# Kernel tuning notes

Hardware: AMD Instinct MI355X
Metric: run time of the kernel (lower is better)

Reference implementation:

```python
import jax, jax.numpy as jnp
import numpy as np

N = 50000      # nodes
E = 800000     # edges (before self loops)
IN_DIM = 256
HID = 64       # per-head hidden dim
HEADS = 4
NEG_SLOPE = 0.2


def setup_inputs() -> dict:
    key = jax.random.key(0)
    k1, k2, k3, k4, k5, k6 = jax.random.split(key, 6)
    x = jax.random.normal(k1, (N, IN_DIM), dtype=jnp.float32)
    edge_index = jax.random.randint(k2, (2, E), 0, N, dtype=jnp.int64)
    # GATConv params (PyG layout): lin weight, att_src, att_dst, bias
    W = jax.random.normal(k3, (IN_DIM, HEADS * HID), dtype=jnp.float32) / np.sqrt(IN_DIM)
    att_src = jax.random.normal(k4, (HEADS, HID), dtype=jnp.float32) / np.sqrt(HID)
    att_dst = jax.random.normal(k5, (HEADS, HID), dtype=jnp.float32) / np.sqrt(HID)
    bias = jnp.zeros((HEADS * HID,), dtype=jnp.float32)
    return {"x": x, "edge_index": edge_index, "W": W,
            "att_src": att_src, "att_dst": att_dst, "bias": bias}


def _gat_forward(x, edge_index, W, att_src, att_dst, bias):
    n = x.shape[0]
    # linear projection per head: [N, H, F]
    h = (x @ W).reshape(n, HEADS, HID)
    # per-node attention logits (computed once on nodes, then gathered)
    a_src = jnp.einsum('nhf,hf->nh', h, att_src)  # [N, H]
    a_dst = jnp.einsum('nhf,hf->nh', h, att_dst)  # [N, H]
    # add self loops (PyG default add_self_loops=True)
    loop = jnp.arange(n, dtype=edge_index.dtype)
    src = jnp.concatenate([edge_index[0], loop])  # [E+N]
    dst = jnp.concatenate([edge_index[1], loop])  # [E+N]
    # edge attention logits with LeakyReLU
    e = jax.nn.leaky_relu(a_src[src] + a_dst[dst], NEG_SLOPE)  # [E+N, H]
    # segment softmax over incoming edges of each destination node
    m = jax.ops.segment_max(e, dst, num_segments=n)            # [N, H]
    num = jnp.exp(e - m[dst])                                  # [E+N, H]
    denom = jax.ops.segment_sum(num, dst, num_segments=n)      # [N, H]
    alpha = num / denom[dst]                                   # [E+N, H]
    # scatter-aggregate weighted source features
    msg = alpha[:, :, None] * h[src]                           # [E+N, H, F]
    out = jax.ops.segment_sum(msg, dst, num_segments=n)        # [N, H, F]
    out = out.reshape(n, HEADS * HID) + bias
    # GraphEncoder.forward: ReLU then Dropout (dropout=0 -> identity)
    return jax.nn.relu(out)


def reference(x, edge_index, W, att_src, att_dst, bias):
    return _gat_forward(x, edge_index, W, att_src, att_dst, bias)
```

## Files before the change

### kernel.cpp

```cpp
#include <hip/hip_runtime.h>
#include <hip/hip_bf16.h>

#define N_NODES 50000
#define N_EDGES 800000
#define TOT_EDGES (N_EDGES + N_NODES)
#define IN_DIM 256
#define OUT_DIM 256
#define HEADS 4
#define NEG_SLOPE 0.2f
#define CAP 96

#define FBLK 256
#define NT   1563
#define LDS_STRIDE 264

typedef __bf16 bf16x8 __attribute__((ext_vector_type(8)));
typedef __bf16 bf16x4 __attribute__((ext_vector_type(4)));
typedef float f32x4 __attribute__((ext_vector_type(4)));

__device__ __forceinline__ float b2f(unsigned short u) {
    union { float f; unsigned int i; } v; v.i = ((unsigned int)u) << 16; return v.f;
}

struct Args {
    const float* x; const int* ei; const float* W;
    const float* att_s; const float* att_d; const float* bias;
    float* out;
    __bf16* Wt; __bf16* h; float* a_src; float* a_dst;
    int* counts; int* ell;
};

__global__ void k_wt(Args A) {
    int k = blockIdx.x;
    int n = threadIdx.x;
    A.Wt[(size_t)n * IN_DIM + k] = (__bf16)A.W[(size_t)k * OUT_DIM + n];
    int idx = blockIdx.x * 256 + threadIdx.x;
    if (idx < N_NODES) A.counts[idx] = 0;
}

__global__ __launch_bounds__(512, 2) void k_gemm_fill(Args A) {
    __shared__ __bf16 xs[32 * LDS_STRIDE];
    __shared__ float  lg[2][8][32];
    const int t = threadIdx.x;

    if (blockIdx.x >= FBLK) {
        const int tile = blockIdx.x - FBLK;
        const int wave = t >> 6;
        const int lane = t & 63;
        const int cc   = lane & 15;
        const int quad = lane >> 4;
        const int n0   = wave * 32;
        const __bf16* __restrict__ Wt = A.Wt;
        const float4* __restrict__ x4 = (const float4*)A.x;

        bf16x8 Bf[8][2];
#pragma unroll
        for (int kk = 0; kk < 8; ++kk)
#pragma unroll
            for (int f = 0; f < 2; ++f)
                Bf[kk][f] = *(const bf16x8*)(Wt
                    + (size_t)(n0 + f * 16 + cc) * IN_DIM + kk * 32 + quad * 8);
        float as0 = A.att_s[n0 + cc], as1 = A.att_s[n0 + 16 + cc];
        float ad0 = A.att_d[n0 + cc], ad1 = A.att_d[n0 + 16 + cc];

        float4 st[4];
#pragma unroll
        for (int i = 0; i < 4; ++i) {
            int f = i * 512 + t;
            int row = f >> 6, c4 = f & 63;
            int grow = tile * 32 + row; if (grow >= N_NODES) grow = N_NODES - 1;
            st[i] = x4[(size_t)grow * 64 + c4];
        }
#pragma unroll
        for (int i = 0; i < 4; ++i) {
            int f = i * 512 + t;
            int row = f >> 6, c4 = f & 63;
            bf16x4 o = { (__bf16)st[i].x, (__bf16)st[i].y, (__bf16)st[i].z, (__bf16)st[i].w };
            *(bf16x4*)&xs[row * LDS_STRIDE + c4 * 4] = o;
        }
        __syncthreads();

        f32x4 acc[2][2];
#pragma unroll
        for (int mt = 0; mt < 2; ++mt)
#pragma unroll
            for (int f = 0; f < 2; ++f) acc[mt][f] = (f32x4){0.f, 0.f, 0.f, 0.f};
#pragma unroll
        for (int kk = 0; kk < 8; ++kk) {
#pragma unroll
            for (int mt = 0; mt < 2; ++mt) {
                bf16x8 a = *(const bf16x8*)&xs[(mt * 16 + cc) * LDS_STRIDE + kk * 32 + quad * 8];
                acc[mt][0] = __builtin_amdgcn_mfma_f32_16x16x32_bf16(a, Bf[kk][0], acc[mt][0], 0, 0, 0);
                acc[mt][1] = __builtin_amdgcn_mfma_f32_16x16x32_bf16(a, Bf[kk][1], acc[mt][1], 0, 0, 0);
            }
        }

#pragma unroll
        for (int mt = 0; mt < 2; ++mt) {
#pragma unroll
            for (int r = 0; r < 4; ++r) {
                float pS = acc[mt][0][r] * as0 + acc[mt][1][r] * as1;
                float pD = acc[mt][0][r] * ad0 + acc[mt][1][r] * ad1;
#pragma unroll
                for (int o = 8; o >= 1; o >>= 1) {
                    pS += __shfl_xor(pS, o, 64);
                    pD += __shfl_xor(pD, o, 64);
                }
                if (cc == 0) {
                    lg[0][wave][mt * 16 + quad * 4 + r] = pS;
                    lg[1][wave][mt * 16 + quad * 4 + r] = pD;
                }
            }
        }
        __syncthreads();

#pragma unroll
        for (int mt = 0; mt < 2; ++mt)
#pragma unroll
            for (int f = 0; f < 2; ++f)
#pragma unroll
                for (int r = 0; r < 4; ++r)
                    xs[(mt * 16 + quad * 4 + r) * LDS_STRIDE + n0 + f * 16 + cc] =
                        (__bf16)acc[mt][f][r];
        if (t < 256) {
            int td = t & 127;
            int row = td >> 2, head = td & 3;
            int grow = tile * 32 + row;
            if (grow < N_NODES) {
                int sd = t >> 7;
                float v = lg[sd][2 * head][row] + lg[sd][2 * head + 1][row];
                float* dst = sd == 0 ? A.a_src : A.a_dst;
                dst[grow * 4 + head] = v;
            }
        }
        __syncthreads();

#pragma unroll
        for (int i = 0; i < 2; ++i) {
            int idx = i * 512 + t;
            int row = idx >> 5, c8 = idx & 31;
            int grow = tile * 32 + row;
            if (grow < N_NODES)
                *(bf16x8*)(A.h + (size_t)grow * OUT_DIM + c8 * 8) =
                    *(const bf16x8*)&xs[row * LDS_STRIDE + c8 * 8];
        }
    } else {
        int nz = 0;
        for (int i = t; i < 1024; i += 512)
            if (A.ei[2 * i + 1] != 0) nz++;
        bool is64 = (__syncthreads_count(nz) == 0);
        const long long* ei64 = (const long long*)A.ei;
        for (int i = blockIdx.x * 512 + t; i < TOT_EDGES; i += FBLK * 512) {
            int s, d;
            if (i < N_EDGES) {
                if (is64) { s = (int)ei64[i]; d = (int)ei64[N_EDGES + i]; }
                else      { s = A.ei[i];      d = A.ei[N_EDGES + i]; }
            } else {
                s = d = i - N_EDGES;
            }
            int pos = atomicAdd(&A.counts[d], 1);
            if (pos < CAP) A.ell[(size_t)d * CAP + pos] = s;
        }
    }
}

__global__ __launch_bounds__(256) void k_agg(Args A) {
    __shared__ float lds_all[4][CAP][4];
    int wave = threadIdx.x >> 6, lane = threadIdx.x & 63;
    int node = blockIdx.x * 4 + wave;
    if (node >= N_NODES) return;
    float (*lds)[4] = lds_all[wave];

    int base = node * CAP;
    int deg  = A.counts[node];
    if (deg > CAP) deg = CAP;
    const float4* as4 = (const float4*)A.a_src;
    float4 ad = ((const float4*)A.a_dst)[node];

    float4 smv = {0.f, 0.f, 0.f, 0.f};
    for (int e = lane; e < deg; e += 64) {
        int s = A.ell[base + e];
        float4 av = as4[s];
        float4 l;
        l.x = av.x + ad.x; l.x = l.x > 0.f ? l.x : NEG_SLOPE * l.x;
        l.y = av.y + ad.y; l.y = l.y > 0.f ? l.y : NEG_SLOPE * l.y;
        l.z = av.z + ad.z; l.z = l.z > 0.f ? l.z : NEG_SLOPE * l.z;
        l.w = av.w + ad.w; l.w = l.w > 0.f ? l.w : NEG_SLOPE * l.w;
        float4 e4;
        e4.x = __expf(l.x); e4.y = __expf(l.y);
        e4.z = __expf(l.z); e4.w = __expf(l.w);
        smv.x += e4.x; smv.y += e4.y; smv.z += e4.z; smv.w += e4.w;
        lds[e][0] = e4.x; lds[e][1] = e4.y; lds[e][2] = e4.z; lds[e][3] = e4.w;
    }
    int padEnd = (deg + 3) & ~3;
    for (int e = deg + lane; e < padEnd; e += 64) {
        lds[e][0] = 0.f; lds[e][1] = 0.f; lds[e][2] = 0.f; lds[e][3] = 0.f;
    }
#pragma unroll
    for (int o = 32; o >= 1; o >>= 1) {
        smv.x += __shfl_xor(smv.x, o, 64);
        smv.y += __shfl_xor(smv.y, o, 64);
        smv.z += __shfl_xor(smv.z, o, 64);
        smv.w += __shfl_xor(smv.w, o, 64);
    }

    int head = lane >> 4;
    float smh = head == 0 ? smv.x : head == 1 ? smv.y : head == 2 ? smv.z : smv.w;
    float inv_d = 1.f / smh;

    float acc0 = 0.f, acc1 = 0.f, acc2 = 0.f, acc3 = 0.f;
    const unsigned short* hs = reinterpret_cast<const unsigned short*>(A.h);
    int rEnd = padEnd;
    for (int e = 0; e < rEnd; e += 4) {
        int s0 = A.ell[base + e];
        int s1 = A.ell[base + ((e + 1 < deg) ? e + 1 : 0)];
        int s2 = A.ell[base + ((e + 2 < deg) ? e + 2 : 0)];
        int s3 = A.ell[base + ((e + 3 < deg) ? e + 3 : 0)];
        float al0 = lds[e][head];
        float al1 = lds[e + 1][head];
        float al2 = lds[e + 2][head];
        float al3 = lds[e + 3][head];
        ushort4 h0 = *(const ushort4*)(hs + (size_t)s0 * OUT_DIM + lane * 4);
        ushort4 h1 = *(const ushort4*)(hs + (size_t)s1 * OUT_DIM + lane * 4);
        ushort4 h2 = *(const ushort4*)(hs + (size_t)s2 * OUT_DIM + lane * 4);
        ushort4 h3 = *(const ushort4*)(hs + (size_t)s3 * OUT_DIM + lane * 4);
        acc0 += al0 * b2f(h0.x) + al1 * b2f(h1.x) + al2 * b2f(h2.x) + al3 * b2f(h3.x);
        acc1 += al0 * b2f(h0.y) + al1 * b2f(h1.y) + al2 * b2f(h2.y) + al3 * b2f(h3.y);
        acc2 += al0 * b2f(h0.z) + al1 * b2f(h1.z) + al2 * b2f(h2.z) + al3 * b2f(h3.z);
        acc3 += al0 * b2f(h0.w) + al1 * b2f(h1.w) + al2 * b2f(h2.w) + al3 * b2f(h3.w);
    }

    float4 bv = ((const float4*)A.bias)[lane];
    f32x4 o4;
    float v0 = acc0 * inv_d + bv.x;
    float v1 = acc1 * inv_d + bv.y;
    float v2 = acc2 * inv_d + bv.z;
    float v3 = acc3 * inv_d + bv.w;
    o4[0] = v0 > 0.f ? v0 : 0.f;
    o4[1] = v1 > 0.f ? v1 : 0.f;
    o4[2] = v2 > 0.f ? v2 : 0.f;
    o4[3] = v3 > 0.f ? v3 : 0.f;
    __builtin_nontemporal_store(o4, (f32x4*)A.out + (size_t)node * 64 + lane);
}

extern "C" void kernel_launch(void* const* d_in, const int* in_sizes, int n_in,
                              void* d_out, int out_size, void* d_ws, size_t ws_size,
                              hipStream_t stream) {
    (void)out_size; (void)ws_size;
    const void* p_x = nullptr; const void* p_ei = nullptr; const void* p_W = nullptr;
    const void* p_small[3] = {nullptr, nullptr, nullptr}; int nsmall = 0;
    for (int i = 0; i < n_in; ++i) {
        switch (in_sizes[i]) {
            case N_NODES * IN_DIM:      p_x = d_in[i]; break;
            case 2 * N_EDGES:           p_ei = d_in[i]; break;
            case IN_DIM * OUT_DIM:      p_W = d_in[i]; break;
            case OUT_DIM:               if (nsmall < 3) p_small[nsmall++] = d_in[i]; break;
            default: break;
        }
    }
    if (!p_x)  p_x  = d_in[0];
    if (!p_ei) p_ei = d_in[1];
    if (!p_W)  p_W  = d_in[2];
    if (nsmall < 3) { p_small[0] = d_in[3]; p_small[1] = d_in[4]; p_small[2] = d_in[5]; }

    char* ws = (char*)d_ws;
    size_t off = 0;
    auto alloc = [&](size_t bytes) -> void* {
        void* p = ws + off;
        off = (off + bytes + 255) & ~(size_t)255;
        return p;
    };
    Args A;
    A.Wt      = (__bf16*)alloc((size_t)IN_DIM * OUT_DIM * 2);
    A.h       = (__bf16*)alloc((size_t)N_NODES * OUT_DIM * 2);
    A.a_src   = (float*)alloc((size_t)N_NODES * HEADS * 4);
    A.a_dst   = (float*)alloc((size_t)N_NODES * HEADS * 4);
    A.counts  = (int*)alloc((size_t)N_NODES * 4);
    A.ell     = (int*)alloc((size_t)N_NODES * CAP * 4);

    A.x     = (const float*)p_x;
    A.ei    = (const int*)p_ei;
    A.W     = (const float*)p_W;
    A.att_s = (const float*)p_small[0];
    A.att_d = (const float*)p_small[1];
    A.bias  = (const float*)p_small[2];
    A.out   = (float*)d_out;

    k_wt<<<dim3(IN_DIM), dim3(OUT_DIM), 0, stream>>>(A);
    k_gemm_fill<<<dim3(FBLK + NT), dim3(512), 0, stream>>>(A);
    k_agg<<<dim3((N_NODES + 3) / 4), dim3(256), 0, stream>>>(A);
}
```

Baseline: 241.7 us.

## Store h head-major and split aggregation per head across blocks

The projected features h are now written in a head-major layout [HEADS][N][64]. The aggregation kernel launches one block group per head, so each wave handles one node and one head. Within a wave, four lane groups each gather a different edge's 128-byte row and are then reduced with shuffles. The aim is a smaller per-head working set for the random gathers, better cache locality, and more parallelism, at the cost of reading the ELL adjacency and computing softmax sums four times per node.

```diff
diff --git a/kernel.cpp b/kernel.cpp
--- a/kernel.cpp
+++ b/kernel.cpp
@@ -12,6 +12,7 @@
 
 #define FBLK 256
 #define NT   1563
+#define NBN  12500
 #define LDS_STRIDE 264
 
 typedef __bf16 bf16x8 __attribute__((ext_vector_type(8)));
@@ -26,7 +27,8 @@
     const float* x; const int* ei; const float* W;
     const float* att_s; const float* att_d; const float* bias;
     float* out;
-    __bf16* Wt; __bf16* h; float* a_src; float* a_dst;
+    __bf16* Wt; __bf16* h;
+    float* a_src; float* a_dst;
     int* counts; int* ell;
 };
 
@@ -139,9 +141,10 @@
         for (int i = 0; i < 2; ++i) {
             int idx = i * 512 + t;
             int row = idx >> 5, c8 = idx & 31;
+            int hd  = c8 >> 3, d8 = c8 & 7;
             int grow = tile * 32 + row;
             if (grow < N_NODES)
-                *(bf16x8*)(A.h + (size_t)grow * OUT_DIM + c8 * 8) =
+                *(bf16x8*)(A.h + ((size_t)hd * N_NODES + grow) * 64 + d8 * 8) =
                     *(const bf16x8*)&xs[row * LDS_STRIDE + c8 * 8];
         }
     } else {
@@ -165,82 +168,65 @@
 }
 
 __global__ __launch_bounds__(256) void k_agg(Args A) {
-    __shared__ float lds_all[4][CAP][4];
-    int wave = threadIdx.x >> 6, lane = threadIdx.x & 63;
-    int node = blockIdx.x * 4 + wave;
+    __shared__ float alp_all[4][CAP];
+    const int wave = threadIdx.x >> 6, lane = threadIdx.x & 63;
+    const int head = blockIdx.x / NBN;
+    const int nb   = blockIdx.x % NBN;
+    const int node = nb * 4 + wave;
     if (node >= N_NODES) return;
-    float (*lds)[4] = lds_all[wave];
-
-    int base = node * CAP;
-    int deg  = A.counts[node];
+    float* alp = alp_all[wave];
+
+    const int base = node * CAP;
+    int deg = A.counts[node];
     if (deg > CAP) deg = CAP;
-    const float4* as4 = (const float4*)A.a_src;
-    float4 ad = ((const float4*)A.a_dst)[node];
-
-    float4 smv = {0.f, 0.f, 0.f, 0.f};
+    const float adh = A.a_dst[node * 4 + head];
+
+    float sm = 0.f;
     for (int e = lane; e < deg; e += 64) {
         int s = A.ell[base + e];
-        float4 av = as4[s];
-        float4 l;
-        l.x = av.x + ad.x; l.x = l.x > 0.f ? l.x : NEG_SLOPE * l.x;
-        l.y = av.y + ad.y; l.y = l.y > 0.f ? l.y : NEG_SLOPE * l.y;
-        l.z = av.z + ad.z; l.z = l.z > 0.f ? l.z : NEG_SLOPE * l.z;
-        l.w = av.w + ad.w; l.w = l.w > 0.f ? l.w : NEG_SLOPE * l.w;
-        float4 e4;
-        e4.x = __expf(l.x); e4.y = __expf(l.y);
-        e4.z = __expf(l.z); e4.w = __expf(l.w);
-        smv.x += e4.x; smv.y += e4.y; smv.z += e4.z; smv.w += e4.w;
-        lds[e][0] = e4.x; lds[e][1] = e4.y; lds[e][2] = e4.z; lds[e][3] = e4.w;
+        float l = A.a_src[s * 4 + head] + adh;
+        l = l > 0.f ? l : NEG_SLOPE * l;
+        float al = __expf(l);
+        sm += al;
+        alp[e] = al;
     }
     int padEnd = (deg + 3) & ~3;
-    for (int e = deg + lane; e < padEnd; e += 64) {
-        lds[e][0] = 0.f; lds[e][1] = 0.f; lds[e][2] = 0.f; lds[e][3] = 0.f;
-    }
-#pragma unroll
-    for (int o = 32; o >= 1; o >>= 1) {
-        smv.x += __shfl_xor(smv.x, o, 64);
-        smv.y += __shfl_xor(smv.y, o, 64);
-        smv.z += __shfl_xor(smv.z, o, 64);
-        smv.w += __shfl_xor(smv.w, o, 64);
-    }
-
-    int head = lane >> 4;
-    float smh = head == 0 ? smv.x : head == 1 ? smv.y : head == 2 ? smv.z : smv.w;
-    float inv_d = 1.f / smh;
-
-    float acc0 = 0.f, acc1 = 0.f, acc2 = 0.f, acc3 = 0.f;
-    const unsigned short* hs = reinterpret_cast<const unsigned short*>(A.h);
-    int rEnd = padEnd;
-    for (int e = 0; e < rEnd; e += 4) {
-        int s0 = A.ell[base + e];
-        int s1 = A.ell[base + ((e + 1 < deg) ? e + 1 : 0)];
-        int s2 = A.ell[base + ((e + 2 < deg) ? e + 2 : 0)];
-        int s3 = A.ell[base + ((e + 3 < deg) ? e + 3 : 0)];
-        float al0 = lds[e][head];
-        float al1 = lds[e + 1][head];
-        float al2 = lds[e + 2][head];
-        float al3 = lds[e + 3][head];
-        ushort4 h0 = *(const ushort4*)(hs + (size_t)s0 * OUT_DIM + lane * 4);
-        ushort4 h1 = *(const ushort4*)(hs + (size_t)s1 * OUT_DIM + lane * 4);
-        ushort4 h2 = *(const ushort4*)(hs + (size_t)s2 * OUT_DIM + lane * 4);
-        ushort4 h3 = *(const ushort4*)(hs + (size_t)s3 * OUT_DIM + lane * 4);
-        acc0 += al0 * b2f(h0.x) + al1 * b2f(h1.x) + al2 * b2f(h2.x) + al3 * b2f(h3.x);
-        acc1 += al0 * b2f(h0.y) + al1 * b2f(h1.y) + al2 * b2f(h2.y) + al3 * b2f(h3.y);
-        acc2 += al0 * b2f(h0.z) + al1 * b2f(h1.z) + al2 * b2f(h2.z) + al3 * b2f(h3.z);
-        acc3 += al0 * b2f(h0.w) + al1 * b2f(h1.w) + al2 * b2f(h2.w) + al3 * b2f(h3.w);
-    }
-
-    float4 bv = ((const float4*)A.bias)[lane];
-    f32x4 o4;
-    float v0 = acc0 * inv_d + bv.x;
-    float v1 = acc1 * inv_d + bv.y;
-    float v2 = acc2 * inv_d + bv.z;
-    float v3 = acc3 * inv_d + bv.w;
-    o4[0] = v0 > 0.f ? v0 : 0.f;
-    o4[1] = v1 > 0.f ? v1 : 0.f;
-    o4[2] = v2 > 0.f ? v2 : 0.f;
-    o4[3] = v3 > 0.f ? v3 : 0.f;
-    __builtin_nontemporal_store(o4, (f32x4*)A.out + (size_t)node * 64 + lane);
+    for (int e = deg + lane; e < padEnd; e += 64) alp[e] = 0.f;
+#pragma unroll
+    for (int o = 32; o >= 1; o >>= 1) sm += __shfl_xor(sm, o, 64);
+    const float inv_d = 1.f / sm;
+
+    const int grp = lane >> 4, d16 = lane & 15;
+    const unsigned short* __restrict__ hH =
+        (const unsigned short*)A.h + (size_t)head * N_NODES * 64;
+    float a0 = 0.f, a1 = 0.f, a2 = 0.f, a3 = 0.f;
+    for (int e0 = 0; e0 < padEnd; e0 += 4) {
+        int e = e0 + grp;
+        int s = (e < deg) ? A.ell[base + e] : 0;
+        float al = alp[e];
+        ushort4 hv = *(const ushort4*)(hH + (size_t)s * 64 + d16 * 4);
+        a0 += al * b2f(hv.x); a1 += al * b2f(hv.y);
+        a2 += al * b2f(hv.z); a3 += al * b2f(hv.w);
+    }
+#pragma unroll
+    for (int o = 32; o >= 16; o >>= 1) {
+        a0 += __shfl_xor(a0, o, 64); a1 += __shfl_xor(a1, o, 64);
+        a2 += __shfl_xor(a2, o, 64); a3 += __shfl_xor(a3, o, 64);
+    }
+    if (grp == 0) {
+        float4 bv = *(const float4*)(A.bias + head * 64 + d16 * 4);
+        float v0 = a0 * inv_d + bv.x;
+        float v1 = a1 * inv_d + bv.y;
+        float v2 = a2 * inv_d + bv.z;
+        float v3 = a3 * inv_d + bv.w;
+        f32x4 o4;
+        o4[0] = v0 > 0.f ? v0 : 0.f;
+        o4[1] = v1 > 0.f ? v1 : 0.f;
+        o4[2] = v2 > 0.f ? v2 : 0.f;
+        o4[3] = v3 > 0.f ? v3 : 0.f;
+        __builtin_nontemporal_store(o4,
+            (f32x4*)(A.out + (size_t)node * OUT_DIM + head * 64) + d16);
+    }
 }
 
 extern "C" void kernel_launch(void* const* d_in, const int* in_sizes, int n_in,
@@ -288,5 +274,5 @@
 
     k_wt<<<dim3(IN_DIM), dim3(OUT_DIM), 0, stream>>>(A);
     k_gemm_fill<<<dim3(FBLK + NT), dim3(512), 0, stream>>>(A);
-    k_agg<<<dim3((N_NODES + 3) / 4), dim3(256), 0, stream>>>(A);
-}
+    k_agg<<<dim3(HEADS * NBN), dim3(256), 0, stream>>>(A);
+}
```

Result: slower. 286.6 us (+18.6%).

## Fuse all three kernels into one persistent cooperative kernel with grid syncs

Applied to the files above, without the earlier changes.

Replaces the three launches (weight transpose/count init, GEMM plus edge fill, aggregation) with a single cooperative persistent kernel that separates phases with grid-wide syncs and loops over tiles and node groups. The aim is to remove launch gaps and tail effects between kernels. In exchange, the ELL fill and the GEMM, which used to run concurrently, now run one after the other. The grid is capped at 1024 blocks, and launch_bounds(512,8) may force register spills in the GEMM phase, which holds 16 bf16x8 B fragments per thread.

```diff
diff --git a/kernel.cpp b/kernel.cpp
--- a/kernel.cpp
+++ b/kernel.cpp
@@ -1,5 +1,8 @@
 #include <hip/hip_runtime.h>
 #include <hip/hip_bf16.h>
+#include <hip/hip_cooperative_groups.h>
+
+namespace cg = cooperative_groups;
 
 #define N_NODES 50000
 #define N_EDGES 800000
@@ -10,7 +13,6 @@
 #define NEG_SLOPE 0.2f
 #define CAP 96
 
-#define FBLK 256
 #define NT   1563
 #define LDS_STRIDE 264
 
@@ -26,131 +28,37 @@
     const float* x; const int* ei; const float* W;
     const float* att_s; const float* att_d; const float* bias;
     float* out;
-    __bf16* Wt; __bf16* h; float* a_src; float* a_dst;
+    __bf16* Wt; __bf16* h;
+    float* a_src; float* a_dst;
     int* counts; int* ell;
 };
 
-__global__ void k_wt(Args A) {
-    int k = blockIdx.x;
-    int n = threadIdx.x;
-    A.Wt[(size_t)n * IN_DIM + k] = (__bf16)A.W[(size_t)k * OUT_DIM + n];
-    int idx = blockIdx.x * 256 + threadIdx.x;
-    if (idx < N_NODES) A.counts[idx] = 0;
-}
-
-__global__ __launch_bounds__(512, 2) void k_gemm_fill(Args A) {
-    __shared__ __bf16 xs[32 * LDS_STRIDE];
-    __shared__ float  lg[2][8][32];
+__global__ __launch_bounds__(512, 8) void k_mega(Args A) {
+    __shared__ __align__(16) unsigned char smem[18944];
+    __bf16* xs = (__bf16*)smem;
+    float (*lg)[8][32] = (float(*)[8][32])(smem + 16896);
+    float (*alds)[CAP][4] = (float(*)[CAP][4])smem;
+
     const int t = threadIdx.x;
-
-    if (blockIdx.x >= FBLK) {
-        const int tile = blockIdx.x - FBLK;
-        const int wave = t >> 6;
-        const int lane = t & 63;
-        const int cc   = lane & 15;
-        const int quad = lane >> 4;
-        const int n0   = wave * 32;
-        const __bf16* __restrict__ Wt = A.Wt;
-        const float4* __restrict__ x4 = (const float4*)A.x;
-
-        bf16x8 Bf[8][2];
-#pragma unroll
-        for (int kk = 0; kk < 8; ++kk)
-#pragma unroll
-            for (int f = 0; f < 2; ++f)
-                Bf[kk][f] = *(const bf16x8*)(Wt
-                    + (size_t)(n0 + f * 16 + cc) * IN_DIM + kk * 32 + quad * 8);
-        float as0 = A.att_s[n0 + cc], as1 = A.att_s[n0 + 16 + cc];
-        float ad0 = A.att_d[n0 + cc], ad1 = A.att_d[n0 + 16 + cc];
-
-        float4 st[4];
-#pragma unroll
-        for (int i = 0; i < 4; ++i) {
-            int f = i * 512 + t;
-            int row = f >> 6, c4 = f & 63;
-            int grow = tile * 32 + row; if (grow >= N_NODES) grow = N_NODES - 1;
-            st[i] = x4[(size_t)grow * 64 + c4];
-        }
-#pragma unroll
-        for (int i = 0; i < 4; ++i) {
-            int f = i * 512 + t;
-            int row = f >> 6, c4 = f & 63;
-            bf16x4 o = { (__bf16)st[i].x, (__bf16)st[i].y, (__bf16)st[i].z, (__bf16)st[i].w };
-            *(bf16x4*)&xs[row * LDS_STRIDE + c4 * 4] = o;
-        }
-        __syncthreads();
-
-        f32x4 acc[2][2];
-#pragma unroll
-        for (int mt = 0; mt < 2; ++mt)
-#pragma unroll
-            for (int f = 0; f < 2; ++f) acc[mt][f] = (f32x4){0.f, 0.f, 0.f, 0.f};
-#pragma unroll
-        for (int kk = 0; kk < 8; ++kk) {
-#pragma unroll
-            for (int mt = 0; mt < 2; ++mt) {
-                bf16x8 a = *(const bf16x8*)&xs[(mt * 16 + cc) * LDS_STRIDE + kk * 32 + quad * 8];
-                acc[mt][0] = __builtin_amdgcn_mfma_f32_16x16x32_bf16(a, Bf[kk][0], acc[mt][0], 0, 0, 0);
-                acc[mt][1] = __builtin_amdgcn_mfma_f32_16x16x32_bf16(a, Bf[kk][1], acc[mt][1], 0, 0, 0);
-            }
-        }
-
-#pragma unroll
-        for (int mt = 0; mt < 2; ++mt) {
-#pragma unroll
-            for (int r = 0; r < 4; ++r) {
-                float pS = acc[mt][0][r] * as0 + acc[mt][1][r] * as1;
-                float pD = acc[mt][0][r] * ad0 + acc[mt][1][r] * ad1;
-#pragma unroll
-                for (int o = 8; o >= 1; o >>= 1) {
-                    pS += __shfl_xor(pS, o, 64);
-                    pD += __shfl_xor(pD, o, 64);
-                }
-                if (cc == 0) {
-                    lg[0][wave][mt * 16 + quad * 4 + r] = pS;
-                    lg[1][wave][mt * 16 + quad * 4 + r] = pD;
-                }
-            }
-        }
-        __syncthreads();
-
-#pragma unroll
-        for (int mt = 0; mt < 2; ++mt)
-#pragma unroll
-            for (int f = 0; f < 2; ++f)
-#pragma unroll
-                for (int r = 0; r < 4; ++r)
-                    xs[(mt * 16 + quad * 4 + r) * LDS_STRIDE + n0 + f * 16 + cc] =
-                        (__bf16)acc[mt][f][r];
-        if (t < 256) {
-            int td = t & 127;
-            int row = td >> 2, head = td & 3;
-            int grow = tile * 32 + row;
-            if (grow < N_NODES) {
-                int sd = t >> 7;
-                float v = lg[sd][2 * head][row] + lg[sd][2 * head + 1][row];
-                float* dst = sd == 0 ? A.a_src : A.a_dst;
-                dst[grow * 4 + head] = v;
-            }
-        }
-        __syncthreads();
-
-#pragma unroll
-        for (int i = 0; i < 2; ++i) {
-            int idx = i * 512 + t;
-            int row = idx >> 5, c8 = idx & 31;
-            int grow = tile * 32 + row;
-            if (grow < N_NODES)
-                *(bf16x8*)(A.h + (size_t)grow * OUT_DIM + c8 * 8) =
-                    *(const bf16x8*)&xs[row * LDS_STRIDE + c8 * 8];
-        }
-    } else {
+    const int wave = t >> 6;
+    const int lane = t & 63;
+    cg::grid_group grid = cg::this_grid();
+
+    for (int idx = blockIdx.x * 512 + t; idx < IN_DIM * OUT_DIM; idx += gridDim.x * 512) {
+        int k = idx >> 8, n = idx & 255;
+        A.Wt[(size_t)n * IN_DIM + k] = (__bf16)A.W[idx];
+    }
+    for (int idx = blockIdx.x * 512 + t; idx < N_NODES; idx += gridDim.x * 512)
+        A.counts[idx] = 0;
+    grid.sync();
+
+    {
         int nz = 0;
         for (int i = t; i < 1024; i += 512)
             if (A.ei[2 * i + 1] != 0) nz++;
         bool is64 = (__syncthreads_count(nz) == 0);
         const long long* ei64 = (const long long*)A.ei;
-        for (int i = blockIdx.x * 512 + t; i < TOT_EDGES; i += FBLK * 512) {
+        for (int i = blockIdx.x * 512 + t; i < TOT_EDGES; i += gridDim.x * 512) {
             int s, d;
             if (i < N_EDGES) {
                 if (is64) { s = (int)ei64[i]; d = (int)ei64[N_EDGES + i]; }
@@ -162,85 +70,187 @@
             if (pos < CAP) A.ell[(size_t)d * CAP + pos] = s;
         }
     }
-}
-
-__global__ __launch_bounds__(256) void k_agg(Args A) {
-    __shared__ float lds_all[4][CAP][4];
-    int wave = threadIdx.x >> 6, lane = threadIdx.x & 63;
-    int node = blockIdx.x * 4 + wave;
-    if (node >= N_NODES) return;
-    float (*lds)[4] = lds_all[wave];
-
-    int base = node * CAP;
-    int deg  = A.counts[node];
-    if (deg > CAP) deg = CAP;
-    const float4* as4 = (const float4*)A.a_src;
-    float4 ad = ((const float4*)A.a_dst)[node];
-
-    float4 smv = {0.f, 0.f, 0.f, 0.f};
-    for (int e = lane; e < deg; e += 64) {
-        int s = A.ell[base + e];
-        float4 av = as4[s];
-        float4 l;
-        l.x = av.x + ad.x; l.x = l.x > 0.f ? l.x : NEG_SLOPE * l.x;
-        l.y = av.y + ad.y; l.y = l.y > 0.f ? l.y : NEG_SLOPE * l.y;
-        l.z = av.z + ad.z; l.z = l.z > 0.f ? l.z : NEG_SLOPE * l.z;
-        l.w = av.w + ad.w; l.w = l.w > 0.f ? l.w : NEG_SLOPE * l.w;
-        float4 e4;
-        e4.x = __expf(l.x); e4.y = __expf(l.y);
-        e4.z = __expf(l.z); e4.w = __expf(l.w);
-        smv.x += e4.x; smv.y += e4.y; smv.z += e4.z; smv.w += e4.w;
-        lds[e][0] = e4.x; lds[e][1] = e4.y; lds[e][2] = e4.z; lds[e][3] = e4.w;
-    }
-    int padEnd = (deg + 3) & ~3;
-    for (int e = deg + lane; e < padEnd; e += 64) {
-        lds[e][0] = 0.f; lds[e][1] = 0.f; lds[e][2] = 0.f; lds[e][3] = 0.f;
-    }
-#pragma unroll
-    for (int o = 32; o >= 1; o >>= 1) {
-        smv.x += __shfl_xor(smv.x, o, 64);
-        smv.y += __shfl_xor(smv.y, o, 64);
-        smv.z += __shfl_xor(smv.z, o, 64);
-        smv.w += __shfl_xor(smv.w, o, 64);
-    }
-
-    int head = lane >> 4;
-    float smh = head == 0 ? smv.x : head == 1 ? smv.y : head == 2 ? smv.z : smv.w;
-    float inv_d = 1.f / smh;
-
-    float acc0 = 0.f, acc1 = 0.f, acc2 = 0.f, acc3 = 0.f;
-    const unsigned short* hs = reinterpret_cast<const unsigned short*>(A.h);
-    int rEnd = padEnd;
-    for (int e = 0; e < rEnd; e += 4) {
-        int s0 = A.ell[base + e];
-        int s1 = A.ell[base + ((e + 1 < deg) ? e + 1 : 0)];
-        int s2 = A.ell[base + ((e + 2 < deg) ? e + 2 : 0)];
-        int s3 = A.ell[base + ((e + 3 < deg) ? e + 3 : 0)];
-        float al0 = lds[e][head];
-        float al1 = lds[e + 1][head];
-        float al2 = lds[e + 2][head];
-        float al3 = lds[e + 3][head];
-        ushort4 h0 = *(const ushort4*)(hs + (size_t)s0 * OUT_DIM + lane * 4);
-        ushort4 h1 = *(const ushort4*)(hs + (size_t)s1 * OUT_DIM + lane * 4);
-        ushort4 h2 = *(const ushort4*)(hs + (size_t)s2 * OUT_DIM + lane * 4);
-        ushort4 h3 = *(const ushort4*)(hs + (size_t)s3 * OUT_DIM + lane * 4);
-        acc0 += al0 * b2f(h0.x) + al1 * b2f(h1.x) + al2 * b2f(h2.x) + al3 * b2f(h3.x);
-        acc1 += al0 * b2f(h0.y) + al1 * b2f(h1.y) + al2 * b2f(h2.y) + al3 * b2f(h3.y);
-        acc2 += al0 * b2f(h0.z) + al1 * b2f(h1.z) + al2 * b2f(h2.z) + al3 * b2f(h3.z);
-        acc3 += al0 * b2f(h0.w) + al1 * b2f(h1.w) + al2 * b2f(h2.w) + al3 * b2f(h3.w);
-    }
-
-    float4 bv = ((const float4*)A.bias)[lane];
-    f32x4 o4;
-    float v0 = acc0 * inv_d + bv.x;
-    float v1 = acc1 * inv_d + bv.y;
-    float v2 = acc2 * inv_d + bv.z;
-    float v3 = acc3 * inv_d + bv.w;
-    o4[0] = v0 > 0.f ? v0 : 0.f;
-    o4[1] = v1 > 0.f ? v1 : 0.f;
-    o4[2] = v2 > 0.f ? v2 : 0.f;
-    o4[3] = v3 > 0.f ? v3 : 0.f;
-    __builtin_nontemporal_store(o4, (f32x4*)A.out + (size_t)node * 64 + lane);
+
+    {
+        const int cc   = lane & 15;
+        const int quad = lane >> 4;
+        const int n0   = wave * 32;
+        const __bf16* __restrict__ Wt = A.Wt;
+        const float4* __restrict__ x4 = (const float4*)A.x;
+
+        bf16x8 Bf[8][2];
+#pragma unroll
+        for (int kk = 0; kk < 8; ++kk)
+#pragma unroll
+            for (int f = 0; f < 2; ++f)
+                Bf[kk][f] = *(const bf16x8*)(Wt
+                    + (size_t)(n0 + f * 16 + cc) * IN_DIM + kk * 32 + quad * 8);
+        float as0 = A.att_s[n0 + cc], as1 = A.att_s[n0 + 16 + cc];
+        float ad0 = A.att_d[n0 + cc], ad1 = A.att_d[n0 + 16 + cc];
+
+        for (int tile = blockIdx.x; tile < NT; tile += gridDim.x) {
+            __syncthreads();
+            float4 st[4];
+#pragma unroll
+            for (int i = 0; i < 4; ++i) {
+                int f = i * 512 + t;
+                int row = f >> 6, c4 = f & 63;
+                int grow = tile * 32 + row; if (grow >= N_NODES) grow = N_NODES - 1;
+                st[i] = x4[(size_t)grow * 64 + c4];
+            }
+#pragma unroll
+            for (int i = 0; i < 4; ++i) {
+                int f = i * 512 + t;
+                int row = f >> 6, c4 = f & 63;
+                bf16x4 o = { (__bf16)st[i].x, (__bf16)st[i].y, (__bf16)st[i].z, (__bf16)st[i].w };
+                *(bf16x4*)&xs[row * LDS_STRIDE + c4 * 4] = o;
+            }
+            __syncthreads();
+
+            f32x4 acc[2][2];
+#pragma unroll
+            for (int mt = 0; mt < 2; ++mt)
+#pragma unroll
+                for (int f = 0; f < 2; ++f) acc[mt][f] = (f32x4){0.f, 0.f, 0.f, 0.f};
+#pragma unroll
+            for (int kk = 0; kk < 8; ++kk) {
+#pragma unroll
+                for (int mt = 0; mt < 2; ++mt) {
+                    bf16x8 a = *(const bf16x8*)&xs[(mt * 16 + cc) * LDS_STRIDE + kk * 32 + quad * 8];
+                    acc[mt][0] = __builtin_amdgcn_mfma_f32_16x16x32_bf16(a, Bf[kk][0], acc[mt][0], 0, 0, 0);
+                    acc[mt][1] = __builtin_amdgcn_mfma_f32_16x16x32_bf16(a, Bf[kk][1], acc[mt][1], 0, 0, 0);
+                }
+            }
+
+#pragma unroll
+            for (int mt = 0; mt < 2; ++mt) {
+#pragma unroll
+                for (int r = 0; r < 4; ++r) {
+                    float pS = acc[mt][0][r] * as0 + acc[mt][1][r] * as1;
+                    float pD = acc[mt][0][r] * ad0 + acc[mt][1][r] * ad1;
+#pragma unroll
+                    for (int o = 8; o >= 1; o >>= 1) {
+                        pS += __shfl_xor(pS, o, 64);
+                        pD += __shfl_xor(pD, o, 64);
+                    }
+                    if (cc == 0) {
+                        lg[0][wave][mt * 16 + quad * 4 + r] = pS;
+                        lg[1][wave][mt * 16 + quad * 4 + r] = pD;
+                    }
+                }
+            }
+            __syncthreads();
+
+#pragma unroll
+            for (int mt = 0; mt < 2; ++mt)
+#pragma unroll
+                for (int f = 0; f < 2; ++f)
+#pragma unroll
+                    for (int r = 0; r < 4; ++r)
+                        xs[(mt * 16 + quad * 4 + r) * LDS_STRIDE + n0 + f * 16 + cc] =
+                            (__bf16)acc[mt][f][r];
+            if (t < 256) {
+                int td = t & 127;
+                int row = td >> 2, head = td & 3;
+                int grow = tile * 32 + row;
+                if (grow < N_NODES) {
+                    int sd = t >> 7;
+                    float v = lg[sd][2 * head][row] + lg[sd][2 * head + 1][row];
+                    float* dst = sd == 0 ? A.a_src : A.a_dst;
+                    dst[grow * 4 + head] = v;
+                }
+            }
+            __syncthreads();
+
+#pragma unroll
+            for (int i = 0; i < 2; ++i) {
+                int idx = i * 512 + t;
+                int row = idx >> 5, c8 = idx & 31;
+                int grow = tile * 32 + row;
+                if (grow < N_NODES)
+                    *(bf16x8*)(A.h + (size_t)grow * OUT_DIM + c8 * 8) =
+                        *(const bf16x8*)&xs[row * LDS_STRIDE + c8 * 8];
+            }
+        }
+    }
+    grid.sync();
+
+    const int ngroups = (N_NODES + 7) / 8;
+    for (int ng = blockIdx.x; ng < ngroups; ng += gridDim.x) {
+        int node = ng * 8 + wave;
+        if (node >= N_NODES) continue;
+        float (*lds)[4] = alds[wave];
+
+        int base = node * CAP;
+        int deg  = A.counts[node];
+        if (deg > CAP) deg = CAP;
+        const float4* as4 = (const float4*)A.a_src;
+        float4 ad = ((const float4*)A.a_dst)[node];
+
+        float4 smv = {0.f, 0.f, 0.f, 0.f};
+        for (int e = lane; e < deg; e += 64) {
+            int s = A.ell[base + e];
+            float4 av = as4[s];
+            float4 l;
+            l.x = av.x + ad.x; l.x = l.x > 0.f ? l.x : NEG_SLOPE * l.x;
+            l.y = av.y + ad.y; l.y = l.y > 0.f ? l.y : NEG_SLOPE * l.y;
+            l.z = av.z + ad.z; l.z = l.z > 0.f ? l.z : NEG_SLOPE * l.z;
+            l.w = av.w + ad.w; l.w = l.w > 0.f ? l.w : NEG_SLOPE * l.w;
+            float4 e4;
+            e4.x = __expf(l.x); e4.y = __expf(l.y);
+            e4.z = __expf(l.z); e4.w = __expf(l.w);
+            smv.x += e4.x; smv.y += e4.y; smv.z += e4.z; smv.w += e4.w;
+            lds[e][0] = e4.x; lds[e][1] = e4.y; lds[e][2] = e4.z; lds[e][3] = e4.w;
+        }
+        int padEnd = (deg + 3) & ~3;
+        for (int e = deg + lane; e < padEnd; e += 64) {
+            lds[e][0] = 0.f; lds[e][1] = 0.f; lds[e][2] = 0.f; lds[e][3] = 0.f;
+        }
+#pragma unroll
+        for (int o = 32; o >= 1; o >>= 1) {
+            smv.x += __shfl_xor(smv.x, o, 64);
+            smv.y += __shfl_xor(smv.y, o, 64);
+            smv.z += __shfl_xor(smv.z, o, 64);
+            smv.w += __shfl_xor(smv.w, o, 64);
+        }
+
+        int head = lane >> 4;
+        float smh = head == 0 ? smv.x : head == 1 ? smv.y : head == 2 ? smv.z : smv.w;
+        float inv_d = 1.f / smh;
+
+        float acc0 = 0.f, acc1 = 0.f, acc2 = 0.f, acc3 = 0.f;
+        const unsigned short* hs = reinterpret_cast<const unsigned short*>(A.h);
+        for (int e = 0; e < padEnd; e += 4) {
+            int s0 = A.ell[base + e];
+            int s1 = A.ell[base + ((e + 1 < deg) ? e + 1 : 0)];
+            int s2 = A.ell[base + ((e + 2 < deg) ? e + 2 : 0)];
+            int s3 = A.ell[base + ((e + 3 < deg) ? e + 3 : 0)];
+            float al0 = lds[e][head];
+            float al1 = lds[e + 1][head];
+            float al2 = lds[e + 2][head];
+            float al3 = lds[e + 3][head];
+            ushort4 h0 = *(const ushort4*)(hs + (size_t)s0 * OUT_DIM + lane * 4);
+            ushort4 h1 = *(const ushort4*)(hs + (size_t)s1 * OUT_DIM + lane * 4);
+            ushort4 h2 = *(const ushort4*)(hs + (size_t)s2 * OUT_DIM + lane * 4);
+            ushort4 h3 = *(const ushort4*)(hs + (size_t)s3 * OUT_DIM + lane * 4);
+            acc0 += al0 * b2f(h0.x) + al1 * b2f(h1.x) + al2 * b2f(h2.x) + al3 * b2f(h3.x);
+            acc1 += al0 * b2f(h0.y) + al1 * b2f(h1.y) + al2 * b2f(h2.y) + al3 * b2f(h3.y);
+            acc2 += al0 * b2f(h0.z) + al1 * b2f(h1.z) + al2 * b2f(h2.z) + al3 * b2f(h3.z);
+            acc3 += al0 * b2f(h0.w) + al1 * b2f(h1.w) + al2 * b2f(h2.w) + al3 * b2f(h3.w);
+        }
+
+        float4 bv = ((const float4*)A.bias)[lane];
+        f32x4 o4;
+        float v0 = acc0 * inv_d + bv.x;
+        float v1 = acc1 * inv_d + bv.y;
+        float v2 = acc2 * inv_d + bv.z;
+        float v3 = acc3 * inv_d + bv.w;
+        o4[0] = v0 > 0.f ? v0 : 0.f;
+        o4[1] = v1 > 0.f ? v1 : 0.f;
+        o4[2] = v2 > 0.f ? v2 : 0.f;
+        o4[3] = v3 > 0.f ? v3 : 0.f;
+        __builtin_nontemporal_store(o4, (f32x4*)A.out + (size_t)node * 64 + lane);
+    }
 }
 
 extern "C" void kernel_launch(void* const* d_in, const int* in_sizes, int n_in,
@@ -286,7 +296,12 @@
     A.bias  = (const float*)p_small[2];
     A.out   = (float*)d_out;
 
-    k_wt<<<dim3(IN_DIM), dim3(OUT_DIM), 0, stream>>>(A);
-    k_gemm_fill<<<dim3(FBLK + NT), dim3(512), 0, stream>>>(A);
-    k_agg<<<dim3((N_NODES + 3) / 4), dim3(256), 0, stream>>>(A);
+    int maxB = 0;
+    hipError_t oe = hipOccupancyMaxActiveBlocksPerMultiprocessor(&maxB, k_mega, 512, 0);
+    int grid = (oe == hipSuccess && maxB > 0) ? maxB * 256 : 512;
+    if (grid > 1024) grid = 1024;
+
+    void* kargs[] = { (void*)&A };
+    hipLaunchCooperativeKernel((const void*)k_mega, dim3(grid), dim3(512),
+                               kargs, 0, stream);
 }
```

Result: slower. 451.0 us (+86.6%).

## Drop weight-transpose kernel, read W directly, unroll aggregation by eight

Applied to the files above, without the earlier changes.

Removes the separate W transpose/convert kernel: GEMM blocks now load fp32 W directly with strided scalar reads and convert to bf16 in registers, and the counts array is zeroed with hipMemsetAsync instead. The aggregation loop pads degree to a multiple of eight and issues eight gathers of h rows before accumulating, to raise memory-level parallelism. The cost is uncoalesced, strided W loads in every GEMM block (1563 blocks each read the 256 KB matrix) and more padding work per node.

```diff
diff --git a/kernel.cpp b/kernel.cpp
--- a/kernel.cpp
+++ b/kernel.cpp
@@ -26,17 +26,9 @@
     const float* x; const int* ei; const float* W;
     const float* att_s; const float* att_d; const float* bias;
     float* out;
-    __bf16* Wt; __bf16* h; float* a_src; float* a_dst;
+    __bf16* h; float* a_src; float* a_dst;
     int* counts; int* ell;
 };
-
-__global__ void k_wt(Args A) {
-    int k = blockIdx.x;
-    int n = threadIdx.x;
-    A.Wt[(size_t)n * IN_DIM + k] = (__bf16)A.W[(size_t)k * OUT_DIM + n];
-    int idx = blockIdx.x * 256 + threadIdx.x;
-    if (idx < N_NODES) A.counts[idx] = 0;
-}
 
 __global__ __launch_bounds__(512, 2) void k_gemm_fill(Args A) {
     __shared__ __bf16 xs[32 * LDS_STRIDE];
@@ -50,16 +42,20 @@
         const int cc   = lane & 15;
         const int quad = lane >> 4;
         const int n0   = wave * 32;
-        const __bf16* __restrict__ Wt = A.Wt;
+        const float* __restrict__ W = A.W;
         const float4* __restrict__ x4 = (const float4*)A.x;
 
         bf16x8 Bf[8][2];
 #pragma unroll
         for (int kk = 0; kk < 8; ++kk)
 #pragma unroll
-            for (int f = 0; f < 2; ++f)
-                Bf[kk][f] = *(const bf16x8*)(Wt
-                    + (size_t)(n0 + f * 16 + cc) * IN_DIM + kk * 32 + quad * 8);
+            for (int f = 0; f < 2; ++f) {
+                const int col = n0 + f * 16 + cc;
+                const int kb  = kk * 32 + quad * 8;
+#pragma unroll
+                for (int j = 0; j < 8; ++j)
+                    Bf[kk][f][j] = (__bf16)W[(size_t)(kb + j) * OUT_DIM + col];
+            }
         float as0 = A.att_s[n0 + cc], as1 = A.att_s[n0 + 16 + cc];
         float ad0 = A.att_d[n0 + cc], ad1 = A.att_d[n0 + 16 + cc];
 
@@ -192,7 +188,7 @@
         smv.x += e4.x; smv.y += e4.y; smv.z += e4.z; smv.w += e4.w;
         lds[e][0] = e4.x; lds[e][1] = e4.y; lds[e][2] = e4.z; lds[e][3] = e4.w;
     }
-    int padEnd = (deg + 3) & ~3;
+    int padEnd = (deg + 7) & ~7;
     for (int e = deg + lane; e < padEnd; e += 64) {
         lds[e][0] = 0.f; lds[e][1] = 0.f; lds[e][2] = 0.f; lds[e][3] = 0.f;
     }
@@ -210,24 +206,25 @@
 
     float acc0 = 0.f, acc1 = 0.f, acc2 = 0.f, acc3 = 0.f;
     const unsigned short* hs = reinterpret_cast<const unsigned short*>(A.h);
-    int rEnd = padEnd;
-    for (int e = 0; e < rEnd; e += 4) {
-        int s0 = A.ell[base + e];
-        int s1 = A.ell[base + ((e + 1 < deg) ? e + 1 : 0)];
-        int s2 = A.ell[base + ((e + 2 < deg) ? e + 2 : 0)];
-        int s3 = A.ell[base + ((e + 3 < deg) ? e + 3 : 0)];
-        float al0 = lds[e][head];
-        float al1 = lds[e + 1][head];
-        float al2 = lds[e + 2][head];
-        float al3 = lds[e + 3][head];
-        ushort4 h0 = *(const ushort4*)(hs + (size_t)s0 * OUT_DIM + lane * 4);
-        ushort4 h1 = *(const ushort4*)(hs + (size_t)s1 * OUT_DIM + lane * 4);
-        ushort4 h2 = *(const ushort4*)(hs + (size_t)s2 * OUT_DIM + lane * 4);
-        ushort4 h3 = *(const ushort4*)(hs + (size_t)s3 * OUT_DIM + lane * 4);
-        acc0 += al0 * b2f(h0.x) + al1 * b2f(h1.x) + al2 * b2f(h2.x) + al3 * b2f(h3.x);
-        acc1 += al0 * b2f(h0.y) + al1 * b2f(h1.y) + al2 * b2f(h2.y) + al3 * b2f(h3.y);
-        acc2 += al0 * b2f(h0.z) + al1 * b2f(h1.z) + al2 * b2f(h2.z) + al3 * b2f(h3.z);
-        acc3 += al0 * b2f(h0.w) + al1 * b2f(h1.w) + al2 * b2f(h2.w) + al3 * b2f(h3.w);
+    for (int e = 0; e < padEnd; e += 8) {
+        int si[8];
+        float al[8];
+        ushort4 hv[8];
+#pragma unroll
+        for (int j = 0; j < 8; ++j) {
+            si[j] = A.ell[base + ((e + j < deg) ? e + j : 0)];
+            al[j] = lds[e + j][head];
+        }
+#pragma unroll
+        for (int j = 0; j < 8; ++j)
+            hv[j] = *(const ushort4*)(hs + (size_t)si[j] * OUT_DIM + lane * 4);
+#pragma unroll
+        for (int j = 0; j < 8; ++j) {
+            acc0 += al[j] * b2f(hv[j].x);
+            acc1 += al[j] * b2f(hv[j].y);
+            acc2 += al[j] * b2f(hv[j].z);
+            acc3 += al[j] * b2f(hv[j].w);
+        }
     }
 
     float4 bv = ((const float4*)A.bias)[lane];
@@ -271,7 +268,6 @@
         return p;
     };
     Args A;
-    A.Wt      = (__bf16*)alloc((size_t)IN_DIM * OUT_DIM * 2);
     A.h       = (__bf16*)alloc((size_t)N_NODES * OUT_DIM * 2);
     A.a_src   = (float*)alloc((size_t)N_NODES * HEADS * 4);
     A.a_dst   = (float*)alloc((size_t)N_NODES * HEADS * 4);
@@ -286,7 +282,7 @@
     A.bias  = (const float*)p_small[2];
     A.out   = (float*)d_out;
 
-    k_wt<<<dim3(IN_DIM), dim3(OUT_DIM), 0, stream>>>(A);
+    hipMemsetAsync(A.counts, 0, (size_t)N_NODES * 4, stream);
     k_gemm_fill<<<dim3(FBLK + NT), dim3(512), 0, stream>>>(A);
     k_agg<<<dim3((N_NODES + 3) / 4), dim3(256), 0, stream>>>(A);
 }
```

New measurement: 248.7 us. 1.03x slower.
